# Kernel optimization log

Measured on AMD Instinct MI355X. Metric: run time of the kernel, lower is better.

Reference implementation:

```python
import jax, jax.numpy as jnp
import numpy as np

HIDDEN = 1024
N_HEADS = 16
HEAD_DIM = HIDDEN // N_HEADS
LN_EPS = 1e-5


def setup_inputs() -> dict:
    key = jax.random.key(0)
    ks = jax.random.split(key, 8)
    B, S = 4, 1024
    inp = {
        'input_tensor': jax.random.normal(ks[0], (B, S, HIDDEN), dtype=jnp.float32),
        'memory_tensor': jax.random.normal(ks[1], (B, S, HIDDEN), dtype=jnp.float32),
        'attention_mask': jnp.ones((B, S, S), dtype=jnp.float32),
        'wq': jax.random.normal(ks[2], (HIDDEN, HIDDEN), dtype=jnp.float32) * 0.02,
        'wk': jax.random.normal(ks[3], (HIDDEN, HIDDEN), dtype=jnp.float32) * 0.02,
        'wv': jax.random.normal(ks[4], (HIDDEN, HIDDEN), dtype=jnp.float32) * 0.02,
        'wo': jax.random.normal(ks[5], (HIDDEN, HIDDEN), dtype=jnp.float32) * 0.02,
        'ln_gamma': jnp.ones((HIDDEN,), dtype=jnp.float32),
        'ln_beta': jnp.zeros((HIDDEN,), dtype=jnp.float32),
        'seq_length': 1024,
        'enc_seq_length': 1024,
    }
    return inp


def _layernorm(x, gamma, beta):
    mu = jnp.mean(x, axis=-1, keepdims=True)
    var = jnp.mean(jnp.square(x - mu), axis=-1, keepdims=True)
    return (x - mu) * jax.lax.rsqrt(var + LN_EPS) * gamma + beta


def reference(input_tensor, memory_tensor, attention_mask, wq, wk, wv, wo,
              ln_gamma, ln_beta, seq_length, enc_seq_length):
    B = input_tensor.shape[0]
    S = seq_length
    x2d = input_tensor.reshape(-1, HIDDEN)            # [B*S, H]
    normed = _layernorm(x2d, ln_gamma, ln_beta)       # LayerPreprocess
    # is_encdec_att=False: memory = normed output (memory_tensor unused)
    mem = normed
    # torch nn.Linear(bias=False): y = x @ W.T
    q = (normed @ wq.T).reshape(B, S, N_HEADS, HEAD_DIM).transpose(0, 2, 1, 3)
    k = (mem @ wk.T).reshape(B, S, N_HEADS, HEAD_DIM).transpose(0, 2, 1, 3)
    v = (mem @ wv.T).reshape(B, S, N_HEADS, HEAD_DIM).transpose(0, 2, 1, 3)
    scale = 1.0 / np.sqrt(float(HEAD_DIM))
    scores = jnp.einsum('bhqd,bhkd->bhqk', q, k) * scale   # [B, H, S, S]
    scores = scores - 10000.0 * (1.0 - attention_mask[:, None, :, :])
    probs = jax.nn.softmax(scores, axis=-1)
    ctx = jnp.einsum('bhqk,bhkd->bhqd', probs, v)          # [B, H, S, dh]
    ctx = ctx.transpose(0, 2, 1, 3).reshape(B * S, HIDDEN)
    attn_out = ctx @ wo.T
    # LayerPostprocess (dropout=0): residual add with raw (pre-LN) input
    return attn_out + x2d
```

## Files before the change

kernel.cpp:

```cpp
#include <hip/hip_runtime.h>
#include <hip/hip_bf16.h>


typedef unsigned short u16;
typedef __attribute__((ext_vector_type(8))) short short8;
typedef __attribute__((ext_vector_type(4))) float f32x4;

__device__ __forceinline__ u16 f2bf(float f) {
  union { float f; unsigned u; } cv; cv.f = f;
  unsigned u = cv.u + 0x7fffu + ((cv.u >> 16) & 1u);
  return (u16)(u >> 16);
}

__device__ __forceinline__ void gload_lds16(const void* g, void* l) {
  __builtin_amdgcn_global_load_lds(
      (const __attribute__((address_space(1))) void*)g,
      (__attribute__((address_space(3))) void*)l, 16, 0, 0);
}

__device__ __forceinline__ f32x4 mfma16(short8 a, short8 b, f32x4 c) {
  return __builtin_amdgcn_mfma_f32_16x16x32_bf16(a, b, c, 0, 0, 0);
}

__global__ __launch_bounds__(256) void ln_kernel(const float* __restrict__ x,
                                                 const float* __restrict__ gamma,
                                                 const float* __restrict__ beta,
                                                 u16* __restrict__ outn) {
  __shared__ float sm[4];
  const int row = blockIdx.x, t = threadIdx.x;
  float4 v = ((const float4*)(x + (size_t)row * 1024))[t];
  float s = v.x + v.y + v.z + v.w;
#pragma unroll
  for (int off = 32; off; off >>= 1) s += __shfl_down(s, off);
  if ((t & 63) == 0) sm[t >> 6] = s;
  __syncthreads();
  const float mu = (sm[0] + sm[1] + sm[2] + sm[3]) * (1.0f / 1024.0f);
  const float dx = v.x - mu, dy = v.y - mu, dz = v.z - mu, dw = v.w - mu;
  float vs = dx * dx + dy * dy + dz * dz + dw * dw;
  __syncthreads();
#pragma unroll
  for (int off = 32; off; off >>= 1) vs += __shfl_down(vs, off);
  if ((t & 63) == 0) sm[t >> 6] = vs;
  __syncthreads();
  const float var = (sm[0] + sm[1] + sm[2] + sm[3]) * (1.0f / 1024.0f);
  const float rstd = rsqrtf(var + 1e-5f);
  float4 g = ((const float4*)gamma)[t];
  float4 b = ((const float4*)beta)[t];
  uint2 pk;
  pk.x = (unsigned)f2bf(dx * rstd * g.x + b.x) | ((unsigned)f2bf(dy * rstd * g.y + b.y) << 16);
  pk.y = (unsigned)f2bf(dz * rstd * g.z + b.z) | ((unsigned)f2bf(dw * rstd * g.w + b.w) << 16);
  *(uint2*)&outn[(size_t)row * 1024 + t * 4] = pk;
}

__global__ __launch_bounds__(256) void cvt_w(const float* __restrict__ wq,
                                             const float* __restrict__ wk,
                                             const float* __restrict__ wv,
                                             const float* __restrict__ wo,
                                             u16* __restrict__ out) {
  const int i = blockIdx.x * 256 + threadIdx.x;
  const int e = i * 4;
  const int seg = e >> 20;
  const int off = e & 1048575;
  const float* src = (seg == 0) ? wq : (seg == 1) ? wk : (seg == 2) ? wv : wo;
  float4 v = *(const float4*)(src + off);
  uint2 pk;
  pk.x = (unsigned)f2bf(v.x) | ((unsigned)f2bf(v.y) << 16);
  pk.y = (unsigned)f2bf(v.z) | ((unsigned)f2bf(v.w) << 16);
  *(uint2*)&out[e] = pk;
}

template <int MODE>
__global__ __launch_bounds__(256) void gemm_bt(const u16* __restrict__ A,
                                               const u16* __restrict__ Bm,
                                               u16* __restrict__ outQ, u16* __restrict__ outK,
                                               u16* __restrict__ outVt,
                                               float* __restrict__ outF,
                                               const float* __restrict__ resid) {
  constexpr int BK = 64, KK = 1024;
  __shared__ u16 As[128 * BK];
  __shared__ u16 Bs[128 * BK];
  const int m0 = blockIdx.y * 128, n0 = blockIdx.x * 128;
  const int t = threadIdx.x;
  const int wid = t >> 6, lane = t & 63;
  const int wm = (wid >> 1) * 64, wn = (wid & 1) * 64;
  const int lr = lane & 15, lg = lane >> 4;
  f32x4 acc[4][4] = {};
  const u16* aSrc = A + (size_t)(m0 + (t >> 3)) * KK + (t & 7) * 8;
  const u16* bSrc = Bm + (size_t)(n0 + (t >> 3)) * KK + (t & 7) * 8;

  for (int k0 = 0; k0 < KK; k0 += BK) {
    __syncthreads();
#pragma unroll
    for (int c = 0; c < 4; c++) {
      gload_lds16(aSrc + (size_t)c * 32 * KK + k0, As + c * 2048 + t * 8);
      gload_lds16(bSrc + (size_t)c * 32 * KK + k0, Bs + c * 2048 + t * 8);
    }
    __syncthreads();
    short8 af[4][2], bfr[4][2];
#pragma unroll
    for (int mi = 0; mi < 4; mi++)
#pragma unroll
      for (int kc = 0; kc < 2; kc++)
        af[mi][kc] = *(const short8*)&As[(wm + mi * 16 + lr) * BK + kc * 32 + lg * 8];
#pragma unroll
    for (int ni = 0; ni < 4; ni++)
#pragma unroll
      for (int kc = 0; kc < 2; kc++)
        bfr[ni][kc] = *(const short8*)&Bs[(wn + ni * 16 + lr) * BK + kc * 32 + lg * 8];
#pragma unroll
    for (int mi = 0; mi < 4; mi++)
#pragma unroll
      for (int ni = 0; ni < 4; ni++)
#pragma unroll
        for (int kc = 0; kc < 2; kc++)
          acc[mi][ni] = mfma16(af[mi][kc], bfr[ni][kc], acc[mi][ni]);
  }

#pragma unroll
  for (int mi = 0; mi < 4; mi++)
#pragma unroll
    for (int ni = 0; ni < 4; ni++)
#pragma unroll
      for (int r = 0; r < 4; r++) {
        const int i = m0 + wm + mi * 16 + lg * 4 + r;
        const int j = n0 + wn + ni * 16 + lr;
        const float val = acc[mi][ni][r];
        if (MODE == 0) {
          const int seg = j >> 10, jj = j & 1023;
          const int h = jj >> 6, d = jj & 63;
          const int b = i >> 10, s_ = i & 1023;
          if (seg == 0)      outQ[((size_t)(b * 16 + h) * 1024 + s_) * 64 + d] = f2bf(val * 0.125f);
          else if (seg == 1) outK[((size_t)(b * 16 + h) * 1024 + s_) * 64 + d] = f2bf(val);
          else               outVt[((size_t)(b * 16 + h) * 64 + d) * 1024 + s_] = f2bf(val);
        } else {
          const size_t o = (size_t)i * 1024 + j;
          outF[o] = val + resid[o];
        }
      }
}

__global__ __launch_bounds__(256) void flash_kernel(const u16* __restrict__ Qg,
                                                    const u16* __restrict__ Kg,
                                                    const u16* __restrict__ Vt,
                                                    const float* __restrict__ mask,
                                                    u16* __restrict__ ctx) {
  const int h = blockIdx.x, qt = blockIdx.y, b = blockIdx.z;
  const int bh = b * 16 + h;
  __shared__ u16 Ks[64 * 64];
  __shared__ u16 Vs[64 * 64];
  __shared__ u16 Ps[4][16 * 64];
  const int t = threadIdx.x, wid = t >> 6, lane = t & 63;
  const int lr = lane & 15, lg = lane >> 4;
  const int hR = lr & 7;
  const int qbase = qt * 64 + wid * 16;

  short8 qf[2];
  {
    const u16* qrow = Qg + ((size_t)bh * 1024 + qbase + lr) * 64;
    qf[0] = *(const short8*)(qrow + lg * 8);
    qf[1] = *(const short8*)(qrow + 32 + lg * 8);
  }
  f32x4 octx[4] = {};
  float m_r[4], l_r[4];
#pragma unroll
  for (int r = 0; r < 4; r++) { m_r[r] = -1e30f; l_r[r] = 0.0f; }

  const u16* kS0 = Kg + (size_t)bh * 65536;
  const u16* vS0 = Vt + (size_t)bh * 65536;
  const int srow = t >> 3;
  const int scb = t & 7;

  const float* mrow[4];
#pragma unroll
  for (int r = 0; r < 4; r++)
    mrow[r] = mask + ((size_t)b * 1024 + qbase + lg * 4 + r) * 1024 + lr;

  for (int kt = 0; kt < 16; kt++) {
    __syncthreads();
#pragma unroll
    for (int c = 0; c < 2; c++) {
      const int row = c * 32 + srow;
      const int sc = (scb ^ (row & 7)) * 8;
      gload_lds16(kS0 + (size_t)(kt * 64 + row) * 64 + sc, Ks + c * 2048 + t * 8);
      gload_lds16(vS0 + (size_t)row * 1024 + kt * 64 + sc, Vs + c * 2048 + t * 8);
    }
    __syncthreads();

    float sv[4][4];
#pragma unroll
    for (int kn = 0; kn < 4; kn++) {
      const int R = kn * 16 + lr;
      short8 kf0 = *(const short8*)&Ks[R * 64 + ((lg ^ hR) << 3)];
      short8 kf1 = *(const short8*)&Ks[R * 64 + (((lg + 4) ^ hR) << 3)];
      f32x4 s = {};
      s = mfma16(qf[0], kf0, s);
      s = mfma16(qf[1], kf1, s);
#pragma unroll
      for (int r = 0; r < 4; r++) {
        const float mv = mrow[r][kn * 16];
        sv[kn][r] = fmaf(10000.0f, mv, s[r]) - 10000.0f;
      }
    }

    float f_r[4];
#pragma unroll
    for (int r = 0; r < 4; r++) {
      float mt = fmaxf(fmaxf(sv[0][r], sv[1][r]), fmaxf(sv[2][r], sv[3][r]));
#pragma unroll
      for (int off = 1; off < 16; off <<= 1) mt = fmaxf(mt, __shfl_xor(mt, off));
      const float mn = fmaxf(m_r[r], mt);
      f_r[r] = __expf(m_r[r] - mn);
      m_r[r] = mn;
      float ps = 0.0f;
#pragma unroll
      for (int kn = 0; kn < 4; kn++) {
        const float p = __expf(sv[kn][r] - mn);
        sv[kn][r] = p;
        ps += p;
      }
#pragma unroll
      for (int off = 1; off < 16; off <<= 1) ps += __shfl_xor(ps, off);
      l_r[r] = l_r[r] * f_r[r] + ps;
    }
#pragma unroll
    for (int g = 0; g < 4; g++)
#pragma unroll
      for (int r = 0; r < 4; r++) octx[g][r] *= f_r[r];

#pragma unroll
    for (int kn = 0; kn < 4; kn++)
#pragma unroll
      for (int r = 0; r < 4; r++) {
        const int row = lg * 4 + r;
        const int kc = kn * 16 + lr;
        Ps[wid][row * 64 + (((kc >> 3) ^ (row & 7)) << 3) + (kc & 7)] = f2bf(sv[kn][r]);
      }

    short8 pa0 = *(const short8*)&Ps[wid][lr * 64 + ((lg ^ hR) << 3)];
    short8 pa1 = *(const short8*)&Ps[wid][lr * 64 + (((lg + 4) ^ hR) << 3)];
#pragma unroll
    for (int g = 0; g < 4; g++) {
      const int R = g * 16 + lr;
      short8 vf0 = *(const short8*)&Vs[R * 64 + ((lg ^ hR) << 3)];
      short8 vf1 = *(const short8*)&Vs[R * 64 + (((lg + 4) ^ hR) << 3)];
      octx[g] = mfma16(pa0, vf0, octx[g]);
      octx[g] = mfma16(pa1, vf1, octx[g]);
    }
#pragma unroll
    for (int r = 0; r < 4; r++) mrow[r] += 64;
  }

#pragma unroll
  for (int g = 0; g < 4; g++)
#pragma unroll
    for (int r = 0; r < 4; r++) {
      const int qr = qbase + lg * 4 + r;
      const float val = octx[g][r] / l_r[r];
      ctx[((size_t)b * 1024 + qr) * 1024 + h * 64 + g * 16 + lr] = f2bf(val);
    }
}

extern "C" void kernel_launch(void* const* d_in, const int* in_sizes, int n_in,
                              void* d_out, int out_size, void* d_ws, size_t ws_size,
                              hipStream_t stream) {
  const float* x     = (const float*)d_in[0];
  const float* mask  = (const float*)d_in[2];
  const float* wq    = (const float*)d_in[3];
  const float* wk    = (const float*)d_in[4];
  const float* wv    = (const float*)d_in[5];
  const float* wo    = (const float*)d_in[6];
  const float* gamma = (const float*)d_in[7];
  const float* beta  = (const float*)d_in[8];
  float* out = (float*)d_out;

  char* ws = (char*)d_ws;
  u16* normed = (u16*)(ws);
  u16* wcat   = (u16*)(ws + (8ull << 20));
  u16* Qg     = (u16*)(ws + (16ull << 20));
  u16* Kg     = (u16*)(ws + (24ull << 20));
  u16* Vtg    = (u16*)(ws + (32ull << 20));
  u16* ctx    = (u16*)(ws + (40ull << 20));
  u16* wo_bf  = wcat + 3072ull * 1024;

  ln_kernel<<<4096, 256, 0, stream>>>(x, gamma, beta, normed);
  cvt_w<<<4096, 256, 0, stream>>>(wq, wk, wv, wo, wcat);
  gemm_bt<0><<<dim3(24, 32), 256, 0, stream>>>(normed, wcat, Qg, Kg, Vtg, nullptr, nullptr);
  flash_kernel<<<dim3(16, 16, 4), 256, 0, stream>>>(Qg, Kg, Vtg, mask, ctx);
  gemm_bt<1><<<dim3(8, 32), 256, 0, stream>>>(ctx, wo_bf, nullptr, nullptr, nullptr, out, x);
}
```

Baseline: 270.1 us.

## Double-buffer K/V in flash kernel and precompute bf16 mask bias

```diff
diff --git a/kernel.cpp b/kernel.cpp
--- a/kernel.cpp
+++ b/kernel.cpp
@@ -10,6 +10,11 @@
   union { float f; unsigned u; } cv; cv.f = f;
   unsigned u = cv.u + 0x7fffu + ((cv.u >> 16) & 1u);
   return (u16)(u >> 16);
+}
+
+__device__ __forceinline__ float bf2f(u16 u) {
+  union { unsigned u; float f; } cv; cv.u = ((unsigned)u) << 16;
+  return cv.f;
 }
 
 __device__ __forceinline__ void gload_lds16(const void* g, void* l) {
@@ -67,6 +72,29 @@
   pk.x = (unsigned)f2bf(v.x) | ((unsigned)f2bf(v.y) << 16);
   pk.y = (unsigned)f2bf(v.z) | ((unsigned)f2bf(v.w) << 16);
   *(uint2*)&out[e] = pk;
+}
+
+__global__ __launch_bounds__(256) void cvt_bias(const float* __restrict__ mask,
+                                                u16* __restrict__ bias) {
+  const int tid = blockIdx.x * 256 + threadIdx.x;
+  const int half = tid & 1;
+  const int lg = (tid >> 1) & 3;
+  const int kt = (tid >> 3) & 15;
+  const int q  = (tid >> 7) & 1023;
+  const int b  = tid >> 17;
+  const float* src = mask + ((size_t)b * 1024 + q) * 1024 + kt * 64 + lg * 4;
+  float4 v0 = *(const float4*)(src + (half * 2 + 0) * 16);
+  float4 v1 = *(const float4*)(src + (half * 2 + 1) * 16);
+  uint4 w;
+  w.x = (unsigned)f2bf(fmaf(10000.f, v0.x, -10000.f)) |
+        ((unsigned)f2bf(fmaf(10000.f, v0.y, -10000.f)) << 16);
+  w.y = (unsigned)f2bf(fmaf(10000.f, v0.z, -10000.f)) |
+        ((unsigned)f2bf(fmaf(10000.f, v0.w, -10000.f)) << 16);
+  w.z = (unsigned)f2bf(fmaf(10000.f, v1.x, -10000.f)) |
+        ((unsigned)f2bf(fmaf(10000.f, v1.y, -10000.f)) << 16);
+  w.w = (unsigned)f2bf(fmaf(10000.f, v1.z, -10000.f)) |
+        ((unsigned)f2bf(fmaf(10000.f, v1.w, -10000.f)) << 16);
+  *(uint4*)&bias[(size_t)tid * 8] = w;
 }
 
 template <int MODE>
@@ -142,121 +170,140 @@
 __global__ __launch_bounds__(256) void flash_kernel(const u16* __restrict__ Qg,
                                                     const u16* __restrict__ Kg,
                                                     const u16* __restrict__ Vt,
-                                                    const float* __restrict__ mask,
+                                                    const u16* __restrict__ bias,
                                                     u16* __restrict__ ctx) {
   const int h = blockIdx.x, qt = blockIdx.y, b = blockIdx.z;
   const int bh = b * 16 + h;
-  __shared__ u16 Ks[64 * 64];
-  __shared__ u16 Vs[64 * 64];
-  __shared__ u16 Ps[4][16 * 64];
+  __shared__ u16 Ks[2][4096];
+  __shared__ u16 Vs[2][4096];
+  __shared__ u16 Ps[4][1024];
   const int t = threadIdx.x, wid = t >> 6, lane = t & 63;
   const int lr = lane & 15, lg = lane >> 4;
   const int hR = lr & 7;
   const int qbase = qt * 64 + wid * 16;
 
-  short8 qf[2];
+  short8 qf0, qf1;
   {
     const u16* qrow = Qg + ((size_t)bh * 1024 + qbase + lr) * 64;
-    qf[0] = *(const short8*)(qrow + lg * 8);
-    qf[1] = *(const short8*)(qrow + 32 + lg * 8);
+    qf0 = *(const short8*)(qrow + lg * 8);
+    qf1 = *(const short8*)(qrow + 32 + lg * 8);
   }
   f32x4 octx[4] = {};
-  float m_r[4], l_r[4];
-#pragma unroll
-  for (int r = 0; r < 4; r++) { m_r[r] = -1e30f; l_r[r] = 0.0f; }
+  float m_ln = -1e30f, l_ln = 0.0f;
 
   const u16* kS0 = Kg + (size_t)bh * 65536;
   const u16* vS0 = Vt + (size_t)bh * 65536;
-  const int srow = t >> 3;
-  const int scb = t & 7;
-
-  const float* mrow[4];
-#pragma unroll
-  for (int r = 0; r < 4; r++)
-    mrow[r] = mask + ((size_t)b * 1024 + qbase + lg * 4 + r) * 1024 + lr;
-
-  for (int kt = 0; kt < 16; kt++) {
-    __syncthreads();
+  const int srow = t >> 3, scb = t & 7;
+
+  const u16* bptr = bias + ((size_t)b * 1024 + qbase + lr) * 1024 + lg * 16;
+
+  auto STAGE = [&](int nb, int kt) {
 #pragma unroll
     for (int c = 0; c < 2; c++) {
       const int row = c * 32 + srow;
       const int sc = (scb ^ (row & 7)) * 8;
-      gload_lds16(kS0 + (size_t)(kt * 64 + row) * 64 + sc, Ks + c * 2048 + t * 8);
-      gload_lds16(vS0 + (size_t)row * 1024 + kt * 64 + sc, Vs + c * 2048 + t * 8);
-    }
-    __syncthreads();
+      gload_lds16(kS0 + (size_t)(kt * 64 + row) * 64 + sc, &Ks[nb][c * 2048 + t * 8]);
+      gload_lds16(vS0 + (size_t)row * 1024 + kt * 64 + sc, &Vs[nb][c * 2048 + t * 8]);
+    }
+  };
+
+  STAGE(0, 0);
+  short8 bc0 = *(const short8*)(bptr);
+  short8 bc1 = *(const short8*)(bptr + 8);
+  asm volatile("s_waitcnt vmcnt(0)" ::: "memory");
+  __builtin_amdgcn_s_barrier();
+  __builtin_amdgcn_sched_barrier(0);
+
+  int cur = 0;
+  for (int kt = 0; kt < 16; kt++) {
+    const int ktn = (kt < 15) ? kt + 1 : 15;
+    STAGE(cur ^ 1, ktn);
+    short8 bn0 = *(const short8*)(bptr + ktn * 64);
+    short8 bn1 = *(const short8*)(bptr + ktn * 64 + 8);
 
     float sv[4][4];
 #pragma unroll
     for (int kn = 0; kn < 4; kn++) {
       const int R = kn * 16 + lr;
-      short8 kf0 = *(const short8*)&Ks[R * 64 + ((lg ^ hR) << 3)];
-      short8 kf1 = *(const short8*)&Ks[R * 64 + (((lg + 4) ^ hR) << 3)];
+      short8 kf0 = *(const short8*)&Ks[cur][R * 64 + ((lg ^ hR) << 3)];
+      short8 kf1 = *(const short8*)&Ks[cur][R * 64 + (((lg + 4) ^ hR) << 3)];
       f32x4 s = {};
-      s = mfma16(qf[0], kf0, s);
-      s = mfma16(qf[1], kf1, s);
-#pragma unroll
-      for (int r = 0; r < 4; r++) {
-        const float mv = mrow[r][kn * 16];
-        sv[kn][r] = fmaf(10000.0f, mv, s[r]) - 10000.0f;
-      }
-    }
-
-    float f_r[4];
-#pragma unroll
-    for (int r = 0; r < 4; r++) {
-      float mt = fmaxf(fmaxf(sv[0][r], sv[1][r]), fmaxf(sv[2][r], sv[3][r]));
-#pragma unroll
-      for (int off = 1; off < 16; off <<= 1) mt = fmaxf(mt, __shfl_xor(mt, off));
-      const float mn = fmaxf(m_r[r], mt);
-      f_r[r] = __expf(m_r[r] - mn);
-      m_r[r] = mn;
-      float ps = 0.0f;
-#pragma unroll
-      for (int kn = 0; kn < 4; kn++) {
-        const float p = __expf(sv[kn][r] - mn);
-        sv[kn][r] = p;
-        ps += p;
-      }
-#pragma unroll
-      for (int off = 1; off < 16; off <<= 1) ps += __shfl_xor(ps, off);
-      l_r[r] = l_r[r] * f_r[r] + ps;
-    }
+      s = mfma16(kf0, qf0, s);
+      s = mfma16(kf1, qf1, s);
+      short8 bsel = (kn < 2) ? bc0 : bc1;
+#pragma unroll
+      for (int r = 0; r < 4; r++)
+        sv[kn][r] = s[r] + bf2f((u16)bsel[(kn & 1) * 4 + r]);
+    }
+
+    float mx0 = fmaxf(fmaxf(sv[0][0], sv[0][1]), fmaxf(sv[0][2], sv[0][3]));
+    float mx1 = fmaxf(fmaxf(sv[1][0], sv[1][1]), fmaxf(sv[1][2], sv[1][3]));
+    float mx2 = fmaxf(fmaxf(sv[2][0], sv[2][1]), fmaxf(sv[2][2], sv[2][3]));
+    float mx3 = fmaxf(fmaxf(sv[3][0], sv[3][1]), fmaxf(sv[3][2], sv[3][3]));
+    float mt = fmaxf(fmaxf(mx0, mx1), fmaxf(mx2, mx3));
+    mt = fmaxf(mt, __shfl_xor(mt, 16));
+    mt = fmaxf(mt, __shfl_xor(mt, 32));
+    const float mn = fmaxf(m_ln, mt);
+    const float f = __expf(m_ln - mn);
+    m_ln = mn;
+    float ps = 0.0f;
+#pragma unroll
+    for (int kn = 0; kn < 4; kn++) {
+      float p0 = __expf(sv[kn][0] - mn), p1 = __expf(sv[kn][1] - mn);
+      float p2 = __expf(sv[kn][2] - mn), p3 = __expf(sv[kn][3] - mn);
+      sv[kn][0] = p0; sv[kn][1] = p1; sv[kn][2] = p2; sv[kn][3] = p3;
+      ps += (p0 + p1) + (p2 + p3);
+    }
+    ps += __shfl_xor(ps, 16);
+    ps += __shfl_xor(ps, 32);
+    l_ln = l_ln * f + ps;
+
+    float fb[4];
+#pragma unroll
+    for (int r = 0; r < 4; r++)
+      fb[r] = __shfl(f, (lane & 48) | (lg * 4 + r), 64);
 #pragma unroll
     for (int g = 0; g < 4; g++)
 #pragma unroll
-      for (int r = 0; r < 4; r++) octx[g][r] *= f_r[r];
-
-#pragma unroll
-    for (int kn = 0; kn < 4; kn++)
-#pragma unroll
-      for (int r = 0; r < 4; r++) {
-        const int row = lg * 4 + r;
-        const int kc = kn * 16 + lr;
-        Ps[wid][row * 64 + (((kc >> 3) ^ (row & 7)) << 3) + (kc & 7)] = f2bf(sv[kn][r]);
-      }
-
-    short8 pa0 = *(const short8*)&Ps[wid][lr * 64 + ((lg ^ hR) << 3)];
-    short8 pa1 = *(const short8*)&Ps[wid][lr * 64 + (((lg + 4) ^ hR) << 3)];
+      for (int r = 0; r < 4; r++) octx[g][r] *= fb[r];
+
+    const int swz = (lr & 7) << 1;
+#pragma unroll
+    for (int kn = 0; kn < 4; kn++) {
+      uint2 w;
+      w.x = (unsigned)f2bf(sv[kn][0]) | ((unsigned)f2bf(sv[kn][1]) << 16);
+      w.y = (unsigned)f2bf(sv[kn][2]) | ((unsigned)f2bf(sv[kn][3]) << 16);
+      *(uint2*)&Ps[wid][lr * 64 + (((kn * 4 + lg) ^ swz) << 2)] = w;
+    }
+    short8 pa0 = *(const short8*)&Ps[wid][lr * 64 + (((2 * lg) ^ swz) << 2)];
+    short8 pa1 = *(const short8*)&Ps[wid][lr * 64 + (((8 + 2 * lg) ^ swz) << 2)];
+
 #pragma unroll
     for (int g = 0; g < 4; g++) {
       const int R = g * 16 + lr;
-      short8 vf0 = *(const short8*)&Vs[R * 64 + ((lg ^ hR) << 3)];
-      short8 vf1 = *(const short8*)&Vs[R * 64 + (((lg + 4) ^ hR) << 3)];
+      short8 vf0 = *(const short8*)&Vs[cur][R * 64 + ((lg ^ hR) << 3)];
+      short8 vf1 = *(const short8*)&Vs[cur][R * 64 + (((lg + 4) ^ hR) << 3)];
       octx[g] = mfma16(pa0, vf0, octx[g]);
       octx[g] = mfma16(pa1, vf1, octx[g]);
     }
-#pragma unroll
-    for (int r = 0; r < 4; r++) mrow[r] += 64;
+
+    asm volatile("s_waitcnt vmcnt(0)" ::: "memory");
+    __builtin_amdgcn_s_barrier();
+    __builtin_amdgcn_sched_barrier(0);
+    cur ^= 1;
+    bc0 = bn0; bc1 = bn1;
   }
 
+  float lb[4];
+#pragma unroll
+  for (int r = 0; r < 4; r++)
+    lb[r] = __shfl(l_ln, (lane & 48) | (lg * 4 + r), 64);
 #pragma unroll
   for (int g = 0; g < 4; g++)
 #pragma unroll
     for (int r = 0; r < 4; r++) {
       const int qr = qbase + lg * 4 + r;
-      const float val = octx[g][r] / l_r[r];
-      ctx[((size_t)b * 1024 + qr) * 1024 + h * 64 + g * 16 + lr] = f2bf(val);
+      ctx[((size_t)b * 1024 + qr) * 1024 + h * 64 + g * 16 + lr] = f2bf(octx[g][r] / lb[r]);
     }
 }
 
@@ -281,10 +328,12 @@
   u16* Vtg    = (u16*)(ws + (32ull << 20));
   u16* ctx    = (u16*)(ws + (40ull << 20));
   u16* wo_bf  = wcat + 3072ull * 1024;
+  u16* bias   = normed;
 
   ln_kernel<<<4096, 256, 0, stream>>>(x, gamma, beta, normed);
   cvt_w<<<4096, 256, 0, stream>>>(wq, wk, wv, wo, wcat);
   gemm_bt<0><<<dim3(24, 32), 256, 0, stream>>>(normed, wcat, Qg, Kg, Vtg, nullptr, nullptr);
-  flash_kernel<<<dim3(16, 16, 4), 256, 0, stream>>>(Qg, Kg, Vtg, mask, ctx);
+  cvt_bias<<<2048, 256, 0, stream>>>(mask, bias);
+  flash_kernel<<<dim3(16, 16, 4), 256, 0, stream>>>(Qg, Kg, Vtg, bias, ctx);
   gemm_bt<1><<<dim3(8, 32), 256, 0, stream>>>(ctx, wo_bf, nullptr, nullptr, nullptr, out, x);
 }
```

Measured after the change: 254.4 us. 1.06x faster.
